# Performance work log

Measured on AMD Instinct MI355X. Metric: run time of the kernel, lower is better.

Reference implementation:

```python
import jax, jax.numpy as jnp
import numpy as np

PRECISION_RATIO = 0.1
ROUTE_THRESH = 0.05

def ternary_quantize(W):
    # TWN-style: delta = 0.7*mean|W|, alpha = mean of kept magnitudes
    delta = 0.7 * jnp.mean(jnp.abs(W))
    mask = (jnp.abs(W) > delta).astype(W.dtype)
    alpha = jnp.sum(jnp.abs(W) * mask) / jnp.maximum(jnp.sum(mask), 1.0)
    return alpha * jnp.sign(W) * mask

def rpb_weight(W, precision_ratio=PRECISION_RATIO):
    # Ternary base + full-precision residual kept for top `precision_ratio` of entries
    Wq = ternary_quantize(W)
    res = W - Wq
    k = max(1, int(precision_ratio * W.size))
    kth = jax.lax.top_k(jnp.abs(res).reshape(-1), k)[0][-1]
    keep = (jnp.abs(res) >= kth).astype(W.dtype)
    return Wq + res * keep

def selective_route(x, threshold=ROUTE_THRESH):
    return x * (jnp.abs(x) >= threshold).astype(x.dtype)

def _lin(x, W, b):
    return x @ W.T + b

def setup_inputs() -> dict:
    key = jax.random.key(0)
    ks = jax.random.split(key, 24)
    B = 8192
    dims = {"vision": 2048, "text": 1024, "audio": 512}
    D = 1024
    T = D * 3  # total_dim = 3072
    s = 0.02
    inp = {
        "x_vision": jax.random.normal(ks[0], (B, dims["vision"]), jnp.float32),
        "x_text": jax.random.normal(ks[1], (B, dims["text"]), jnp.float32),
        "x_audio": jax.random.normal(ks[2], (B, dims["audio"]), jnp.float32),
        "Wv": jax.random.normal(ks[3], (D, dims["vision"]), jnp.float32) * s,
        "bv": jnp.zeros((D,), jnp.float32),
        "Wt": jax.random.normal(ks[4], (D, dims["text"]), jnp.float32) * s,
        "bt": jnp.zeros((D,), jnp.float32),
        "Wa": jax.random.normal(ks[5], (D, dims["audio"]), jnp.float32) * s,
        "ba": jnp.zeros((D,), jnp.float32),
        "Wq1": jax.random.normal(ks[6], (D, T), jnp.float32) * s,
        "bq1": jnp.zeros((D,), jnp.float32),
        "Wq2": jax.random.normal(ks[7], (D, D), jnp.float32) * s,
        "bq2": jnp.zeros((D,), jnp.float32),
        "Wf1": jax.random.normal(ks[8], (D, T), jnp.float32) * s,
        "bf1": jnp.zeros((D,), jnp.float32),
        "Wf2": jax.random.normal(ks[9], (D, D), jnp.float32) * s,
        "bf2": jnp.zeros((D,), jnp.float32),
        "mix_ratio": jnp.asarray(0.75, jnp.float32),
    }
    return inp

def reference(x_vision, x_text, x_audio, Wv, bv, Wt, bt, Wa, ba,
              Wq1, bq1, Wq2, bq2, Wf1, bf1, Wf2, bf2, mix_ratio):
    # per-modality projections then concat in modality order
    pv = _lin(x_vision, Wv, bv)
    pt = _lin(x_text, Wt, bt)
    pa = _lin(x_audio, Wa, ba)
    concat = jnp.concatenate([pv, pt, pa], axis=1)  # [B, 3*D]
    routed = selective_route(concat)
    # quantized (RPB) branch
    h = jax.nn.relu(_lin(routed, rpb_weight(Wq1), bq1))
    out_quant = _lin(h, rpb_weight(Wq2), bq2)
    # full-precision branch
    g = jax.nn.relu(_lin(concat, Wf1, bf1))
    out_full = _lin(g, Wf2, bf2)
    mix = jax.nn.sigmoid(mix_ratio)
    return mix * out_quant + (1.0 - mix) * out_full
```

## Files before the change

kernel.cpp:

```cpp
#include <hip/hip_runtime.h>


typedef _Float16 f16x8 __attribute__((ext_vector_type(8)));
typedef float f32x4 __attribute__((ext_vector_type(4)));

__device__ __forceinline__ unsigned short f16b(float v) {
  union { _Float16 h; unsigned short u; } cv; cv.h = (_Float16)v; return cv.u;
}

__device__ __forceinline__ void load_lds16(const void* g, void* l) {
  __builtin_amdgcn_global_load_lds(
      (const __attribute__((address_space(1))) void*)g,
      (__attribute__((address_space(3))) void*)l, 16, 0, 0);
}

__device__ __forceinline__ float sigmoidf_dev(float x) {
  return 1.0f / (1.0f + expf(-x));
}

__device__ __forceinline__ float reduce_region_f(const float* part, int lo, int hi,
                                                 float* sbuf) {
  float a = 0.f;
  for (int i = lo + threadIdx.x; i < hi; i += 256) a += part[i];
  sbuf[threadIdx.x] = a; __syncthreads();
  for (int o = 128; o > 0; o >>= 1) {
    if ((int)threadIdx.x < o) sbuf[threadIdx.x] += sbuf[threadIdx.x + o];
    __syncthreads();
  }
  float r = sbuf[0];
  __syncthreads();
  return r;
}

struct F2HArgs {
  const float* src[7];
  unsigned short* dst[7];
  long cum4[8];
};

__global__ void f2h_all(F2HArgs a) {
  long total = a.cum4[7];
  for (long i = (long)blockIdx.x * blockDim.x + threadIdx.x; i < total;
       i += (long)gridDim.x * blockDim.x) {
    int s = 0;
#pragma unroll
    for (int j = 1; j < 7; ++j) s += (i >= a.cum4[j]) ? 1 : 0;
    long off = i - a.cum4[s];
    float4 v = ((const float4*)a.src[s])[off];
    ushort4 o;
    o.x = f16b(v.x); o.y = f16b(v.y); o.z = f16b(v.z); o.w = f16b(v.w);
    ((ushort4*)a.dst[s])[off] = o;
  }
}

#define NB_W1 768
#define NB_TOT 1024

__global__ void part_abssum2(const float* __restrict__ W1, long n41,
                             const float* __restrict__ W2, long n42,
                             float* __restrict__ part, unsigned* __restrict__ hist) {
  __shared__ float s[256];
  if (blockIdx.x < 2) hist[blockIdx.x * 256 + threadIdx.x] = 0;
  int w = blockIdx.x < NB_W1 ? 0 : 1;
  const float4* W4 = (const float4*)(w ? W2 : W1);
  long n4 = w ? n42 : n41;
  int nb = w ? (NB_TOT - NB_W1) : NB_W1;
  int bid = w ? (int)blockIdx.x - NB_W1 : (int)blockIdx.x;
  float acc = 0.f;
  for (long i = (long)bid * blockDim.x + threadIdx.x; i < n4;
       i += (long)nb * blockDim.x) {
    float4 v = W4[i];
    acc += fabsf(v.x) + fabsf(v.y) + fabsf(v.z) + fabsf(v.w);
  }
  s[threadIdx.x] = acc; __syncthreads();
  for (int o = 128; o > 0; o >>= 1) {
    if ((int)threadIdx.x < o) s[threadIdx.x] += s[threadIdx.x + o];
    __syncthreads();
  }
  if (threadIdx.x == 0) part[blockIdx.x] = s[0];
}

__global__ void part_kept2(const float* __restrict__ W1, long S1,
                           const float* __restrict__ W2, long S2,
                           const float* __restrict__ part,
                           float* __restrict__ scal,
                           float* __restrict__ pb, unsigned* __restrict__ pc) {
  __shared__ float sf[256]; __shared__ unsigned sc[256];
  int w = blockIdx.x < NB_W1 ? 0 : 1;
  const float* W = w ? W2 : W1;
  long S = w ? S2 : S1;
  int nb = w ? (NB_TOT - NB_W1) : NB_W1;
  int bid = w ? (int)blockIdx.x - NB_W1 : (int)blockIdx.x;
  float tot = reduce_region_f(part, w ? NB_W1 : 0, w ? NB_TOT : NB_W1, sf);
  float delta = 0.7f * (tot / (float)S);
  if (bid == 0 && threadIdx.x == 0) scal[w * 2] = delta;
  float a = 0.f; unsigned c = 0;
  for (long i = (long)bid * blockDim.x + threadIdx.x; i < S;
       i += (long)nb * blockDim.x) {
    float aw = fabsf(W[i]);
    if (aw > delta) { a += aw; ++c; }
  }
  sf[threadIdx.x] = a; sc[threadIdx.x] = c; __syncthreads();
  for (int o = 128; o > 0; o >>= 1) {
    if ((int)threadIdx.x < o) { sf[threadIdx.x] += sf[threadIdx.x + o]; sc[threadIdx.x] += sc[threadIdx.x + o]; }
    __syncthreads();
  }
  if (threadIdx.x == 0) { pb[blockIdx.x] = sf[0]; pc[blockIdx.x] = sc[0]; }
}

__global__ void fin_alpha(const float* __restrict__ pb, const unsigned* __restrict__ pc,
                          float* __restrict__ scal) {
  __shared__ float sf[256]; __shared__ unsigned sc[256];
  int w = blockIdx.x;
  int lo = w ? NB_W1 : 0, hi = w ? NB_TOT : NB_W1;
  float a = 0.f; unsigned c = 0;
  for (int i = lo + threadIdx.x; i < hi; i += 256) { a += pb[i]; c += pc[i]; }
  sf[threadIdx.x] = a; sc[threadIdx.x] = c; __syncthreads();
  for (int o = 128; o > 0; o >>= 1) {
    if ((int)threadIdx.x < o) { sf[threadIdx.x] += sf[threadIdx.x + o]; sc[threadIdx.x] += sc[threadIdx.x + o]; }
    __syncthreads();
  }
  if (threadIdx.x == 0) {
    float cnt = (float)sc[0]; if (cnt < 1.f) cnt = 1.f;
    scal[w * 2 + 1] = sf[0] / cnt;
  }
}

__global__ void hist_pass2(const float* __restrict__ W1, long S1,
                           const float* __restrict__ W2, long S2,
                           const float* __restrict__ scal,
                           const unsigned* __restrict__ u,
                           unsigned* __restrict__ hist, int shift) {
  __shared__ unsigned h[256];
  h[threadIdx.x] = 0; __syncthreads();
  int w = blockIdx.x < NB_W1 ? 0 : 1;
  const float* W = w ? W2 : W1;
  long S = w ? S2 : S1;
  int nb = w ? (NB_TOT - NB_W1) : NB_W1;
  int bid = w ? (int)blockIdx.x - NB_W1 : (int)blockIdx.x;
  float delta = scal[w * 2], alpha = scal[w * 2 + 1];
  unsigned prefix = (shift >= 24) ? 0u : u[w * 4];
  int hs = shift + 8;
  for (long i = (long)bid * blockDim.x + threadIdx.x; i < S;
       i += (long)nb * blockDim.x) {
    float x = W[i];
    float aw = fabsf(x);
    float wq = (aw > delta) ? copysignf(alpha, x) : 0.0f;
    unsigned ub = __float_as_uint(fabsf(x - wq));
    bool ok = (hs >= 32) || ((ub >> hs) == (prefix >> hs));
    if (ok) atomicAdd(&h[(ub >> shift) & 255u], 1u);
  }
  __syncthreads();
  if (h[threadIdx.x]) atomicAdd(&hist[w * 256 + threadIdx.x], h[threadIdx.x]);
}

__global__ void sel_pass2(unsigned* __restrict__ hist, unsigned* __restrict__ u,
                          int shift, int first, int last,
                          unsigned k1, unsigned k2) {
  __shared__ unsigned h[256];
  int w = blockIdx.x, t = threadIdx.x;
  h[t] = hist[w * 256 + t];
  __syncthreads();
  if (t == 0) {
    unsigned krem = first ? (w ? k2 : k1) : u[w * 4 + 1];
    unsigned cum = 0, above = 0;
    int bstar = 0;
    for (int b = 255; b >= 0; --b) {
      unsigned nc = cum + h[b];
      if (nc >= krem) { bstar = b; above = cum; break; }
      cum = nc;
    }
    unsigned np = ((unsigned)bstar) << shift;
    u[w * 4 + 0] = first ? np : (u[w * 4 + 0] | np);
    u[w * 4 + 1] = krem - above;
    if (last) u[w * 4 + 2] = first ? np : u[w * 4 + 0];
  }
  __syncthreads();
  hist[w * 256 + t] = 0;
}

struct FinArgs {
  const float* Wq1; const float* Wq2; const float* Wf2;
  const float* bq2; const float* bf2; const float* mixp;
  const float* scal;
  const unsigned* u;
  unsigned short* wq1_h;
  unsigned short* w2_h;
  float* b2;
};

__global__ void finalize_weights(FinArgs a) {
  const long S1 = 3145728, S2 = 1048576, D = 1024;
  float mix = sigmoidf_dev(a.mixp[0]);
  long total = S1 + 2 * S2 + D;
  float d1 = a.scal[0], a1 = a.scal[1];
  float d2 = a.scal[2], a2 = a.scal[3];
  unsigned kth1 = a.u[2], kth2 = a.u[6];
  for (long i = (long)blockIdx.x * blockDim.x + threadIdx.x; i < total;
       i += (long)gridDim.x * blockDim.x) {
    if (i < S1) {
      float x = a.Wq1[i];
      float wq = (fabsf(x) > d1) ? copysignf(a1, x) : 0.0f;
      float res = x - wq;
      float v = wq + ((__float_as_uint(fabsf(res)) >= kth1) ? res : 0.0f);
      a.wq1_h[i] = f16b(v);
    } else if (i < S1 + S2) {
      long j = i - S1; int r = (int)(j >> 10), c = (int)(j & 1023);
      float x = a.Wq2[j];
      float wq = (fabsf(x) > d2) ? copysignf(a2, x) : 0.0f;
      float res = x - wq;
      float v = wq + ((__float_as_uint(fabsf(res)) >= kth2) ? res : 0.0f);
      a.w2_h[(long)r * 2048 + c] = f16b(mix * v);
    } else if (i < S1 + 2 * S2) {
      long j = i - S1 - S2; int r = (int)(j >> 10), c = (int)(j & 1023);
      a.w2_h[(long)r * 2048 + 1024 + c] = f16b((1.0f - mix) * a.Wf2[j]);
    } else {
      long j = i - S1 - 2 * S2;
      a.b2[j] = mix * a.bq2[j] + (1.0f - mix) * a.bf2[j];
    }
  }
}

struct GemmArgs {
  const unsigned short* A0; const unsigned short* A1; const unsigned short* A2;
  const unsigned short* B0; const unsigned short* B1; const unsigned short* B2;
  const float* c0; const float* c1; const float* c2;
  int K0, K1, K2;
  int nrows;
  int ldc;
  unsigned short* o0; unsigned short* o1; float* oF;
};

template <int EPI>
__global__ __launch_bounds__(512) void gemm6(GemmArgs g) {
  constexpr int AL = 128 * 32 * 2;
  constexpr int BL = 256 * 32 * 2;
  __shared__ __align__(16) char sm[2 * AL + 2 * BL];
  const int tid = threadIdx.x;
  const int wid = tid >> 6;
  const int lane = tid & 63;
  const int wm = wid >> 2, wn = wid & 3;

  const int nwg = gridDim.x;
  const int id = (blockIdx.x & 7) * (nwg >> 3) + (blockIdx.x >> 3);
  const int ncols = nwg / g.nrows;
  const int c = id % ncols, r = id / ncols;
  const int sel = c >> 2, lc = c & 3;

  const unsigned short* A = sel == 0 ? g.A0 : (sel == 1 ? g.A1 : g.A2);
  const unsigned short* Bw = sel == 0 ? g.B0 : (sel == 1 ? g.B1 : g.B2);
  const float* bias = sel == 0 ? g.c0 : (sel == 1 ? g.c1 : g.c2);
  const int K = sel == 0 ? g.K0 : (sel == 1 ? g.K1 : g.K2);
  const long brow = (long)r * 128;
  const int bRowB = lc * 256;

  f32x4 acc[4][4];
#pragma unroll
  for (int i = 0; i < 4; ++i)
#pragma unroll
    for (int j = 0; j < 4; ++j)
#pragma unroll
      for (int e = 0; e < 4; ++e) acc[i][j][e] = 0.f;

  const int oA = tid * 16;
  const unsigned short* aSrc = A + (brow + (oA >> 6)) * (long)K + ((oA & 63) >> 1);
  const unsigned short* bSrc[2];
#pragma unroll
  for (int j = 0; j < 2; ++j) {
    int o = j * 8192 + tid * 16;
    bSrc[j] = Bw + (long)(bRowB + (o >> 6)) * K + ((o & 63) >> 1);
  }

  auto STAGE = [&](int buf, int k0) {
    load_lds16(aSrc + k0, sm + (size_t)buf * AL + wid * 1024);
#pragma unroll
    for (int j = 0; j < 2; ++j)
      load_lds16(bSrc[j] + k0, sm + 2 * AL + (size_t)buf * BL + j * 8192 + wid * 1024);
  };

  const int kb = (lane >> 4) * 16;
  auto COMPUTE = [&](int buf) {
    const char* lAp = sm + (size_t)buf * AL;
    const char* lBp = sm + 2 * AL + (size_t)buf * BL;
    f16x8 a[4], b[4];
#pragma unroll
    for (int m = 0; m < 4; ++m)
      a[m] = *(const f16x8*)(lAp + (wm * 64 + m * 16 + (lane & 15)) * 64 + kb);
#pragma unroll
    for (int n = 0; n < 4; ++n)
      b[n] = *(const f16x8*)(lBp + (wn * 64 + n * 16 + (lane & 15)) * 64 + kb);
#pragma unroll
    for (int m = 0; m < 4; ++m)
#pragma unroll
      for (int n = 0; n < 4; ++n)
        acc[m][n] = __builtin_amdgcn_mfma_f32_16x16x32_f16(a[m], b[n], acc[m][n], 0, 0, 0);
  };

  const int NT = K >> 5;
  STAGE(0, 0);
  __syncthreads();
  int cur = 0;
  for (int t = 0; t < NT - 1; ++t) {
    STAGE(cur ^ 1, (t + 1) << 5);
    COMPUTE(cur);
    __syncthreads();
    cur ^= 1;
  }
  COMPUTE(cur);

  const int cb = c * 256 + wn * 64;
  const int rb = r * 128 + wm * 64;
  const int bcol0 = bRowB + wn * 64;
#pragma unroll
  for (int i = 0; i < 4; ++i) {
    int r0 = rb + i * 16 + ((lane >> 4) << 2);
#pragma unroll
    for (int j = 0; j < 4; ++j) {
      int ccol = cb + j * 16 + (lane & 15);
      float bb = bias[bcol0 + j * 16 + (lane & 15)];
#pragma unroll
      for (int e = 0; e < 4; ++e) {
        float v = acc[i][j][e] + bb;
        long idx = (long)(r0 + e) * g.ldc + ccol;
        if constexpr (EPI == 0) {
          g.o0[idx] = f16b(v);
          g.o1[idx] = f16b(fabsf(v) >= 0.05f ? v : 0.0f);
        } else if constexpr (EPI == 1) {
          g.o0[idx] = f16b(fmaxf(v, 0.0f));
        } else {
          g.oF[idx] = v;
        }
      }
    }
  }
}

extern "C" void kernel_launch(void* const* d_in, const int* in_sizes, int n_in,
                              void* d_out, int out_size, void* d_ws, size_t ws_size,
                              hipStream_t stream) {
  const float* xv = (const float*)d_in[0];
  const float* xt = (const float*)d_in[1];
  const float* xa = (const float*)d_in[2];
  const float* Wv = (const float*)d_in[3];
  const float* bv = (const float*)d_in[4];
  const float* Wt = (const float*)d_in[5];
  const float* bt = (const float*)d_in[6];
  const float* Wa = (const float*)d_in[7];
  const float* ba = (const float*)d_in[8];
  const float* Wq1 = (const float*)d_in[9];
  const float* bq1 = (const float*)d_in[10];
  const float* Wq2 = (const float*)d_in[11];
  const float* bq2 = (const float*)d_in[12];
  const float* Wf1 = (const float*)d_in[13];
  const float* bf1 = (const float*)d_in[14];
  const float* Wf2 = (const float*)d_in[15];
  const float* bf2 = (const float*)d_in[16];
  const float* mixp = (const float*)d_in[17];

  const int B = 8192, D = 1024, T = 3072;
  const int Kv = 2048, Kt = 1024, Ka = 512;
  const long S1 = (long)D * T, S2 = (long)D * D;

  char* w = (char*)d_ws;
  auto alloc = [&](size_t bytes) -> char* {
    char* p = w; w += (bytes + 255) & ~(size_t)255; return p;
  };
  unsigned short* xv_h = (unsigned short*)alloc((size_t)B * Kv * 2);
  unsigned short* xt_h = (unsigned short*)alloc((size_t)B * Kt * 2);
  unsigned short* xa_h = (unsigned short*)alloc((size_t)B * Ka * 2);
  unsigned short* wv_h = (unsigned short*)alloc((size_t)D * Kv * 2);
  unsigned short* wt_h = (unsigned short*)alloc((size_t)D * Kt * 2);
  unsigned short* wa_h = (unsigned short*)alloc((size_t)D * Ka * 2);
  unsigned short* wq1_h = (unsigned short*)alloc((size_t)D * T * 2);
  unsigned short* wf1_h = (unsigned short*)alloc((size_t)D * T * 2);
  unsigned short* w2_h = (unsigned short*)alloc((size_t)D * 2048 * 2);
  unsigned short* concat_h = (unsigned short*)alloc((size_t)B * T * 2);
  unsigned short* routed_h = (unsigned short*)alloc((size_t)B * T * 2);
  unsigned short* a2_h = (unsigned short*)alloc((size_t)B * 2048 * 2);
  float* b2 = (float*)alloc(D * 4);
  float* part = (float*)alloc(1024 * 4);
  float* pb = (float*)alloc(1024 * 4);
  unsigned* pc = (unsigned*)alloc(1024 * 4);
  float* scal = (float*)alloc(64);
  unsigned* u = (unsigned*)alloc(64);
  unsigned* hist = (unsigned*)alloc(2 * 256 * 4);

  F2HArgs fa;
  fa.src[0] = xv;  fa.dst[0] = xv_h;
  fa.src[1] = xt;  fa.dst[1] = xt_h;
  fa.src[2] = xa;  fa.dst[2] = xa_h;
  fa.src[3] = Wv;  fa.dst[3] = wv_h;
  fa.src[4] = Wt;  fa.dst[4] = wt_h;
  fa.src[5] = Wa;  fa.dst[5] = wa_h;
  fa.src[6] = Wf1; fa.dst[6] = wf1_h;
  long n4s[7] = {(long)B * Kv / 4, (long)B * Kt / 4, (long)B * Ka / 4,
                 (long)D * Kv / 4, (long)D * Kt / 4, (long)D * Ka / 4, S1 / 4};
  fa.cum4[0] = 0;
  for (int i = 0; i < 7; ++i) fa.cum4[i + 1] = fa.cum4[i] + n4s[i];
  f2h_all<<<2048, 256, 0, stream>>>(fa);

  part_abssum2<<<NB_TOT, 256, 0, stream>>>(Wq1, S1 / 4, Wq2, S2 / 4, part, hist);
  part_kept2<<<NB_TOT, 256, 0, stream>>>(Wq1, S1, Wq2, S2, part, scal, pb, pc);
  fin_alpha<<<2, 256, 0, stream>>>(pb, pc, scal);
  for (int rr = 0; rr < 4; ++rr) {
    hist_pass2<<<NB_TOT, 256, 0, stream>>>(Wq1, S1, Wq2, S2, scal, u, hist, 24 - 8 * rr);
    sel_pass2<<<2, 256, 0, stream>>>(hist, u, 24 - 8 * rr, rr == 0 ? 1 : 0,
                                     rr == 3 ? 1 : 0,
                                     (unsigned)(S1 / 10), (unsigned)(S2 / 10));
  }

  FinArgs fw;
  fw.Wq1 = Wq1; fw.Wq2 = Wq2; fw.Wf2 = Wf2;
  fw.bq2 = bq2; fw.bf2 = bf2; fw.mixp = mixp;
  fw.scal = scal; fw.u = u;
  fw.wq1_h = wq1_h; fw.w2_h = w2_h; fw.b2 = b2;
  finalize_weights<<<1024, 256, 0, stream>>>(fw);

  GemmArgs gp;
  gp.A0 = xv_h; gp.A1 = xt_h; gp.A2 = xa_h;
  gp.B0 = wv_h; gp.B1 = wt_h; gp.B2 = wa_h;
  gp.c0 = bv; gp.c1 = bt; gp.c2 = ba;
  gp.K0 = Kv; gp.K1 = Kt; gp.K2 = Ka;
  gp.nrows = B / 128; gp.ldc = T;
  gp.o0 = concat_h; gp.o1 = routed_h; gp.oF = nullptr;
  gemm6<0><<<12 * (B / 128), 512, 0, stream>>>(gp);

  GemmArgs gh;
  gh.A0 = routed_h; gh.A1 = concat_h; gh.A2 = routed_h;
  gh.B0 = wq1_h; gh.B1 = wf1_h; gh.B2 = wq1_h;
  gh.c0 = bq1; gh.c1 = bf1; gh.c2 = bq1;
  gh.K0 = T; gh.K1 = T; gh.K2 = T;
  gh.nrows = B / 128; gh.ldc = 2048;
  gh.o0 = a2_h; gh.o1 = nullptr; gh.oF = nullptr;
  gemm6<1><<<8 * (B / 128), 512, 0, stream>>>(gh);

  GemmArgs gf;
  gf.A0 = a2_h; gf.A1 = a2_h; gf.A2 = a2_h;
  gf.B0 = w2_h; gf.B1 = w2_h; gf.B2 = w2_h;
  gf.c0 = b2; gf.c1 = b2; gf.c2 = b2;
  gf.K0 = 2048; gf.K1 = 2048; gf.K2 = 2048;
  gf.nrows = B / 128; gf.ldc = D;
  gf.o0 = nullptr; gf.o1 = nullptr; gf.oF = (float*)d_out;
  gemm6<2><<<4 * (B / 128), 512, 0, stream>>>(gf);
}
```

Measured before the change: 424.3 us.

## Triple-buffer GEMM pipeline and fold scalar/select kernels into histogram passes

The GEMM moves from double to triple buffering of LDS tiles. Explicit vmcnt waits and one barrier per k-step let loads two tiles ahead overlap compute. The tiny fin_alpha and sel_pass kernels are removed: each histogram pass and the finalize kernel recompute delta, alpha and the radix prefix from per-round histograms, which cuts kernel launches and serialization. Finalize grid size is doubled. This raises LDS use per block (possibly lowering occupancy) and adds redundant reductions in every block.

```diff
diff --git a/kernel.cpp b/kernel.cpp
--- a/kernel.cpp
+++ b/kernel.cpp
@@ -17,6 +17,9 @@
 __device__ __forceinline__ float sigmoidf_dev(float x) {
   return 1.0f / (1.0f + expf(-x));
 }
+
+#define NB_W1 768
+#define NB_TOT 1024
 
 __device__ __forceinline__ float reduce_region_f(const float* part, int lo, int hi,
                                                  float* sbuf) {
@@ -32,6 +35,37 @@
   return r;
 }
 
+__device__ __forceinline__ float alpha_region(const float* pb, const unsigned* pc,
+                                              int lo, int hi, float* sf, unsigned* sc) {
+  float a = 0.f; unsigned c = 0;
+  for (int i = lo + threadIdx.x; i < hi; i += 256) { a += pb[i]; c += pc[i]; }
+  sf[threadIdx.x] = a; sc[threadIdx.x] = c; __syncthreads();
+  for (int o = 128; o > 0; o >>= 1) {
+    if ((int)threadIdx.x < o) { sf[threadIdx.x] += sf[threadIdx.x + o]; sc[threadIdx.x] += sc[threadIdx.x + o]; }
+    __syncthreads();
+  }
+  float s = sf[0]; float cnt = (float)sc[0];
+  __syncthreads();
+  if (cnt < 1.f) cnt = 1.f;
+  return s / cnt;
+}
+
+__device__ unsigned radix_chain(const unsigned* hists, int w, int nr, unsigned k) {
+  unsigned prefix = 0, krem = k;
+  for (int rr = 0; rr < nr; ++rr) {
+    const unsigned* h = hists + (rr * 2 + w) * 256;
+    unsigned cum = 0, above = 0; int bstar = 0;
+    for (int b = 255; b >= 0; --b) {
+      unsigned nc = cum + h[b];
+      if (nc >= krem) { bstar = b; above = cum; break; }
+      cum = nc;
+    }
+    prefix |= ((unsigned)bstar) << (24 - 8 * rr);
+    krem -= above;
+  }
+  return prefix;
+}
+
 struct F2HArgs {
   const float* src[7];
   unsigned short* dst[7];
@@ -53,14 +87,10 @@
   }
 }
 
-#define NB_W1 768
-#define NB_TOT 1024
-
 __global__ void part_abssum2(const float* __restrict__ W1, long n41,
                              const float* __restrict__ W2, long n42,
-                             float* __restrict__ part, unsigned* __restrict__ hist) {
+                             float* __restrict__ part) {
   __shared__ float s[256];
-  if (blockIdx.x < 2) hist[blockIdx.x * 256 + threadIdx.x] = 0;
   int w = blockIdx.x < NB_W1 ? 0 : 1;
   const float4* W4 = (const float4*)(w ? W2 : W1);
   long n4 = w ? n42 : n41;
@@ -83,7 +113,6 @@
 __global__ void part_kept2(const float* __restrict__ W1, long S1,
                            const float* __restrict__ W2, long S2,
                            const float* __restrict__ part,
-                           float* __restrict__ scal,
                            float* __restrict__ pb, unsigned* __restrict__ pc) {
   __shared__ float sf[256]; __shared__ unsigned sc[256];
   int w = blockIdx.x < NB_W1 ? 0 : 1;
@@ -93,7 +122,6 @@
   int bid = w ? (int)blockIdx.x - NB_W1 : (int)blockIdx.x;
   float tot = reduce_region_f(part, w ? NB_W1 : 0, w ? NB_TOT : NB_W1, sf);
   float delta = 0.7f * (tot / (float)S);
-  if (bid == 0 && threadIdx.x == 0) scal[w * 2] = delta;
   float a = 0.f; unsigned c = 0;
   for (long i = (long)bid * blockDim.x + threadIdx.x; i < S;
        i += (long)nb * blockDim.x) {
@@ -108,38 +136,29 @@
   if (threadIdx.x == 0) { pb[blockIdx.x] = sf[0]; pc[blockIdx.x] = sc[0]; }
 }
 
-__global__ void fin_alpha(const float* __restrict__ pb, const unsigned* __restrict__ pc,
-                          float* __restrict__ scal) {
+__global__ void hist_pass_r(const float* __restrict__ W1, long S1,
+                            const float* __restrict__ W2, long S2,
+                            const float* __restrict__ part,
+                            const float* __restrict__ pb, const unsigned* __restrict__ pc,
+                            unsigned* __restrict__ hists, int round,
+                            unsigned k1, unsigned k2) {
   __shared__ float sf[256]; __shared__ unsigned sc[256];
-  int w = blockIdx.x;
-  int lo = w ? NB_W1 : 0, hi = w ? NB_TOT : NB_W1;
-  float a = 0.f; unsigned c = 0;
-  for (int i = lo + threadIdx.x; i < hi; i += 256) { a += pb[i]; c += pc[i]; }
-  sf[threadIdx.x] = a; sc[threadIdx.x] = c; __syncthreads();
-  for (int o = 128; o > 0; o >>= 1) {
-    if ((int)threadIdx.x < o) { sf[threadIdx.x] += sf[threadIdx.x + o]; sc[threadIdx.x] += sc[threadIdx.x + o]; }
-    __syncthreads();
-  }
-  if (threadIdx.x == 0) {
-    float cnt = (float)sc[0]; if (cnt < 1.f) cnt = 1.f;
-    scal[w * 2 + 1] = sf[0] / cnt;
-  }
-}
-
-__global__ void hist_pass2(const float* __restrict__ W1, long S1,
-                           const float* __restrict__ W2, long S2,
-                           const float* __restrict__ scal,
-                           const unsigned* __restrict__ u,
-                           unsigned* __restrict__ hist, int shift) {
   __shared__ unsigned h[256];
-  h[threadIdx.x] = 0; __syncthreads();
+  __shared__ unsigned spfx;
   int w = blockIdx.x < NB_W1 ? 0 : 1;
   const float* W = w ? W2 : W1;
   long S = w ? S2 : S1;
   int nb = w ? (NB_TOT - NB_W1) : NB_W1;
   int bid = w ? (int)blockIdx.x - NB_W1 : (int)blockIdx.x;
-  float delta = scal[w * 2], alpha = scal[w * 2 + 1];
-  unsigned prefix = (shift >= 24) ? 0u : u[w * 4];
+  int lo = w ? NB_W1 : 0, hi = w ? NB_TOT : NB_W1;
+  float tot = reduce_region_f(part, lo, hi, sf);
+  float delta = 0.7f * (tot / (float)S);
+  float alpha = alpha_region(pb, pc, lo, hi, sf, sc);
+  if (threadIdx.x == 0) spfx = radix_chain(hists, w, round, w ? k2 : k1);
+  h[threadIdx.x] = 0;
+  __syncthreads();
+  unsigned prefix = spfx;
+  int shift = 24 - 8 * round;
   int hs = shift + 8;
   for (long i = (long)bid * blockDim.x + threadIdx.x; i < S;
        i += (long)nb * blockDim.x) {
@@ -151,51 +170,38 @@
     if (ok) atomicAdd(&h[(ub >> shift) & 255u], 1u);
   }
   __syncthreads();
-  if (h[threadIdx.x]) atomicAdd(&hist[w * 256 + threadIdx.x], h[threadIdx.x]);
-}
-
-__global__ void sel_pass2(unsigned* __restrict__ hist, unsigned* __restrict__ u,
-                          int shift, int first, int last,
-                          unsigned k1, unsigned k2) {
-  __shared__ unsigned h[256];
-  int w = blockIdx.x, t = threadIdx.x;
-  h[t] = hist[w * 256 + t];
-  __syncthreads();
-  if (t == 0) {
-    unsigned krem = first ? (w ? k2 : k1) : u[w * 4 + 1];
-    unsigned cum = 0, above = 0;
-    int bstar = 0;
-    for (int b = 255; b >= 0; --b) {
-      unsigned nc = cum + h[b];
-      if (nc >= krem) { bstar = b; above = cum; break; }
-      cum = nc;
-    }
-    unsigned np = ((unsigned)bstar) << shift;
-    u[w * 4 + 0] = first ? np : (u[w * 4 + 0] | np);
-    u[w * 4 + 1] = krem - above;
-    if (last) u[w * 4 + 2] = first ? np : u[w * 4 + 0];
-  }
-  __syncthreads();
-  hist[w * 256 + t] = 0;
+  if (h[threadIdx.x]) atomicAdd(&hists[(round * 2 + w) * 256 + threadIdx.x], h[threadIdx.x]);
 }
 
 struct FinArgs {
   const float* Wq1; const float* Wq2; const float* Wf2;
   const float* bq2; const float* bf2; const float* mixp;
-  const float* scal;
-  const unsigned* u;
+  const float* part; const float* pb; const unsigned* pc;
+  const unsigned* hists;
+  unsigned k1, k2;
   unsigned short* wq1_h;
   unsigned short* w2_h;
   float* b2;
 };
 
 __global__ void finalize_weights(FinArgs a) {
+  __shared__ float sf[256]; __shared__ unsigned sc[256];
+  __shared__ unsigned sk1, sk2;
   const long S1 = 3145728, S2 = 1048576, D = 1024;
+  float tot1 = reduce_region_f(a.part, 0, NB_W1, sf);
+  float d1 = 0.7f * (tot1 / (float)S1);
+  float tot2 = reduce_region_f(a.part, NB_W1, NB_TOT, sf);
+  float d2 = 0.7f * (tot2 / (float)S2);
+  float a1 = alpha_region(a.pb, a.pc, 0, NB_W1, sf, sc);
+  float a2 = alpha_region(a.pb, a.pc, NB_W1, NB_TOT, sf, sc);
+  if (threadIdx.x == 0) {
+    sk1 = radix_chain(a.hists, 0, 4, a.k1);
+    sk2 = radix_chain(a.hists, 1, 4, a.k2);
+  }
+  __syncthreads();
+  unsigned kth1 = sk1, kth2 = sk2;
   float mix = sigmoidf_dev(a.mixp[0]);
   long total = S1 + 2 * S2 + D;
-  float d1 = a.scal[0], a1 = a.scal[1];
-  float d2 = a.scal[2], a2 = a.scal[3];
-  unsigned kth1 = a.u[2], kth2 = a.u[6];
   for (long i = (long)blockIdx.x * blockDim.x + threadIdx.x; i < total;
        i += (long)gridDim.x * blockDim.x) {
     if (i < S1) {
@@ -232,10 +238,11 @@
 };
 
 template <int EPI>
-__global__ __launch_bounds__(512) void gemm6(GemmArgs g) {
+__global__ __launch_bounds__(512) void gemm7(GemmArgs g) {
   constexpr int AL = 128 * 32 * 2;
   constexpr int BL = 256 * 32 * 2;
-  __shared__ __align__(16) char sm[2 * AL + 2 * BL];
+  constexpr int TL = AL + BL;
+  __shared__ __align__(16) char sm[3 * TL];
   const int tid = threadIdx.x;
   const int wid = tid >> 6;
   const int lane = tid & 63;
@@ -272,16 +279,16 @@
   }
 
   auto STAGE = [&](int buf, int k0) {
-    load_lds16(aSrc + k0, sm + (size_t)buf * AL + wid * 1024);
-#pragma unroll
-    for (int j = 0; j < 2; ++j)
-      load_lds16(bSrc[j] + k0, sm + 2 * AL + (size_t)buf * BL + j * 8192 + wid * 1024);
+    char* base = sm + (size_t)buf * TL;
+    load_lds16(aSrc + k0, base + wid * 1024);
+    load_lds16(bSrc[0] + k0, base + AL + wid * 1024);
+    load_lds16(bSrc[1] + k0, base + AL + 8192 + wid * 1024);
   };
 
   const int kb = (lane >> 4) * 16;
   auto COMPUTE = [&](int buf) {
-    const char* lAp = sm + (size_t)buf * AL;
-    const char* lBp = sm + 2 * AL + (size_t)buf * BL;
+    const char* lAp = sm + (size_t)buf * TL;
+    const char* lBp = lAp + AL;
     f16x8 a[4], b[4];
 #pragma unroll
     for (int m = 0; m < 4; ++m)
@@ -298,15 +305,22 @@
 
   const int NT = K >> 5;
   STAGE(0, 0);
-  __syncthreads();
-  int cur = 0;
-  for (int t = 0; t < NT - 1; ++t) {
-    STAGE(cur ^ 1, (t + 1) << 5);
+  STAGE(1, 32);
+  int cur = 0, nxt2 = 2;
+  for (int t = 0; t < NT; ++t) {
+    if (t + 1 < NT) {
+      asm volatile("s_waitcnt vmcnt(3)" ::: "memory");
+    } else {
+      asm volatile("s_waitcnt vmcnt(0)" ::: "memory");
+    }
+    __builtin_amdgcn_s_barrier();
+    __builtin_amdgcn_sched_barrier(0);
+    asm volatile("" ::: "memory");
+    if (t + 2 < NT) STAGE(nxt2, (t + 2) << 5);
     COMPUTE(cur);
-    __syncthreads();
-    cur ^= 1;
-  }
-  COMPUTE(cur);
+    cur = (cur == 2) ? 0 : cur + 1;
+    nxt2 = (nxt2 == 2) ? 0 : nxt2 + 1;
+  }
 
   const int cb = c * 256 + wn * 64;
   const int rb = r * 128 + wm * 64;
@@ -381,9 +395,11 @@
   float* part = (float*)alloc(1024 * 4);
   float* pb = (float*)alloc(1024 * 4);
   unsigned* pc = (unsigned*)alloc(1024 * 4);
-  float* scal = (float*)alloc(64);
-  unsigned* u = (unsigned*)alloc(64);
-  unsigned* hist = (unsigned*)alloc(2 * 256 * 4);
+  unsigned* hists = (unsigned*)alloc(4 * 2 * 256 * 4);
+
+  const unsigned k1 = (unsigned)(S1 / 10), k2 = (unsigned)(S2 / 10);
+
+  hipMemsetAsync(hists, 0, 4 * 2 * 256 * 4, stream);
 
   F2HArgs fa;
   fa.src[0] = xv;  fa.dst[0] = xv_h;
@@ -399,22 +415,19 @@
   for (int i = 0; i < 7; ++i) fa.cum4[i + 1] = fa.cum4[i] + n4s[i];
   f2h_all<<<2048, 256, 0, stream>>>(fa);
 
-  part_abssum2<<<NB_TOT, 256, 0, stream>>>(Wq1, S1 / 4, Wq2, S2 / 4, part, hist);
-  part_kept2<<<NB_TOT, 256, 0, stream>>>(Wq1, S1, Wq2, S2, part, scal, pb, pc);
-  fin_alpha<<<2, 256, 0, stream>>>(pb, pc, scal);
-  for (int rr = 0; rr < 4; ++rr) {
-    hist_pass2<<<NB_TOT, 256, 0, stream>>>(Wq1, S1, Wq2, S2, scal, u, hist, 24 - 8 * rr);
-    sel_pass2<<<2, 256, 0, stream>>>(hist, u, 24 - 8 * rr, rr == 0 ? 1 : 0,
-                                     rr == 3 ? 1 : 0,
-                                     (unsigned)(S1 / 10), (unsigned)(S2 / 10));
-  }
+  part_abssum2<<<NB_TOT, 256, 0, stream>>>(Wq1, S1 / 4, Wq2, S2 / 4, part);
+  part_kept2<<<NB_TOT, 256, 0, stream>>>(Wq1, S1, Wq2, S2, part, pb, pc);
+  for (int rr = 0; rr < 4; ++rr)
+    hist_pass_r<<<NB_TOT, 256, 0, stream>>>(Wq1, S1, Wq2, S2, part, pb, pc,
+                                            hists, rr, k1, k2);
 
   FinArgs fw;
   fw.Wq1 = Wq1; fw.Wq2 = Wq2; fw.Wf2 = Wf2;
   fw.bq2 = bq2; fw.bf2 = bf2; fw.mixp = mixp;
-  fw.scal = scal; fw.u = u;
+  fw.part = part; fw.pb = pb; fw.pc = pc; fw.hists = hists;
+  fw.k1 = k1; fw.k2 = k2;
   fw.wq1_h = wq1_h; fw.w2_h = w2_h; fw.b2 = b2;
-  finalize_weights<<<1024, 256, 0, stream>>>(fw);
+  finalize_weights<<<2048, 256, 0, stream>>>(fw);
 
   GemmArgs gp;
   gp.A0 = xv_h; gp.A1 = xt_h; gp.A2 = xa_h;
@@ -423,7 +436,7 @@
   gp.K0 = Kv; gp.K1 = Kt; gp.K2 = Ka;
   gp.nrows = B / 128; gp.ldc = T;
   gp.o0 = concat_h; gp.o1 = routed_h; gp.oF = nullptr;
-  gemm6<0><<<12 * (B / 128), 512, 0, stream>>>(gp);
+  gemm7<0><<<12 * (B / 128), 512, 0, stream>>>(gp);
 
   GemmArgs gh;
   gh.A0 = routed_h; gh.A1 = concat_h; gh.A2 = routed_h;
@@ -432,7 +445,7 @@
   gh.K0 = T; gh.K1 = T; gh.K2 = T;
   gh.nrows = B / 128; gh.ldc = 2048;
   gh.o0 = a2_h; gh.o1 = nullptr; gh.oF = nullptr;
-  gemm6<1><<<8 * (B / 128), 512, 0, stream>>>(gh);
+  gemm7<1><<<8 * (B / 128), 512, 0, stream>>>(gh);
 
   GemmArgs gf;
   gf.A0 = a2_h; gf.A1 = a2_h; gf.A2 = a2_h;
@@ -441,5 +454,5 @@
   gf.K0 = 2048; gf.K1 = 2048; gf.K2 = 2048;
   gf.nrows = B / 128; gf.ldc = D;
   gf.o0 = nullptr; gf.o1 = nullptr; gf.oF = (float*)d_out;
-  gemm6<2><<<4 * (B / 128), 512, 0, stream>>>(gf);
-}
+  gemm7<2><<<4 * (B / 128), 512, 0, stream>>>(gf);
+}
```

New measurement: 477.8 us. 12.6% more time.
